# Optimization experiments

Hardware: AMD Instinct MI355X
Metric: run time of the kernel (lower is better)

The kernel has to match this reference:

```python
import jax, jax.numpy as jnp
import numpy as np

N_NODES = 100000
NEG_SLOPE = 0.01  # F.leaky_relu default


def _gin_mean_layer(x, src, dst):
    """DGL GINConv(aggregator='mean', apply_func=None, eps=0, activation=leaky_relu).
    out = leaky_relu((1+eps)*x + mean_{in-neighbors} x_src), nodes with no in-edges get mean=0.
    """
    msg_sum = jax.ops.segment_sum(x[src], dst, num_segments=N_NODES)  # [N, D]
    deg = jax.ops.segment_sum(jnp.ones(src.shape, dtype=x.dtype), dst, num_segments=N_NODES)  # [N]
    mean = msg_sum / jnp.maximum(deg, 1.0)[:, None]
    return jax.nn.leaky_relu(x + mean, negative_slope=NEG_SLOPE)


def setup_inputs() -> dict:
    key = jax.random.key(0)
    k0, k1, k2, k3, k4 = jax.random.split(key, 5)
    n_edges = 640000
    d = 128
    return {
        "node_features": jax.random.normal(k0, (N_NODES, d), dtype=jnp.float32),
        "edges1_src": jax.random.randint(k1, (n_edges,), 0, N_NODES, dtype=jnp.int64),
        "edges1_dst": jax.random.randint(k2, (n_edges,), 0, N_NODES, dtype=jnp.int64),
        "edges2_src": jax.random.randint(k3, (n_edges,), 0, N_NODES, dtype=jnp.int64),
        "edges2_dst": jax.random.randint(k4, (n_edges,), 0, N_NODES, dtype=jnp.int64),
    }


def reference(node_features, edges1_src, edges1_dst, edges2_src, edges2_dst):
    h_AC1 = _gin_mean_layer(node_features, edges1_src, edges1_dst)
    h_CA1 = _gin_mean_layer(node_features, edges2_src, edges2_dst)
    h = jnp.concatenate((h_AC1, h_CA1), axis=1)  # [N, 2D]
    h_AC2 = _gin_mean_layer(h, edges1_src, edges1_dst)
    h_CA2 = _gin_mean_layer(h, edges2_src, edges2_dst)
    return jnp.concatenate((h_AC2, h_CA2), axis=1)  # [N, 4D]
```

## Files before the change

kernel.cpp:

```cpp
#include <hip/hip_runtime.h>

#define N_NODES 100000
#define NEG 0.01f
#define CAP 32
#define EDGE_ILP 8

typedef float f4v __attribute__((ext_vector_type(4)));

__device__ __forceinline__ float lrelu(float v) { return v > 0.f ? v : NEG * v; }

__device__ __forceinline__ unsigned int f2bf(float f) {
    unsigned int x = __float_as_uint(f);
    return (x + 0x7fffu + ((x >> 16) & 1u)) >> 16;
}
__device__ __forceinline__ unsigned int pack2bf(float lo, float hi) {
    return f2bf(lo) | (f2bf(hi) << 16);
}
__device__ __forceinline__ float bf_lo(unsigned int u) { return __uint_as_float(u << 16); }
__device__ __forceinline__ float bf_hi(unsigned int u) { return __uint_as_float(u & 0xffff0000u); }

__device__ __forceinline__ void unpack8(uint4 u, float* f) {
    f[0] = bf_lo(u.x); f[1] = bf_hi(u.x);
    f[2] = bf_lo(u.y); f[3] = bf_hi(u.y);
    f[4] = bf_lo(u.z); f[5] = bf_hi(u.z);
    f[6] = bf_lo(u.w); f[7] = bf_hi(u.w);
}

__device__ __forceinline__ unsigned int packq(float v, int sh) {
    float c = fminf(fmaxf(v * 16.f, -127.f), 127.f);
    int q = __float2int_rn(c);
    return ((unsigned int)(q & 255)) << sh;
}
__device__ __forceinline__ uint2 pack8i8(const float* f) {
    uint2 r;
    r.x = packq(f[0], 0) | packq(f[1], 8) | packq(f[2], 16) | packq(f[3], 24);
    r.y = packq(f[4], 0) | packq(f[5], 8) | packq(f[6], 16) | packq(f[7], 24);
    return r;
}
__device__ __forceinline__ void addsext8(uint2 u, int* acc) {
    acc[0] += ((int)(u.x << 24)) >> 24;
    acc[1] += ((int)(u.x << 16)) >> 24;
    acc[2] += ((int)(u.x <<  8)) >> 24;
    acc[3] += ((int)u.x) >> 24;
    acc[4] += ((int)(u.y << 24)) >> 24;
    acc[5] += ((int)(u.y << 16)) >> 24;
    acc[6] += ((int)(u.y <<  8)) >> 24;
    acc[7] += ((int)u.y) >> 24;
}

__global__ void __launch_bounds__(256) build_and_convert(
        const int* __restrict__ s1, const int* __restrict__ d1a, int E1,
        const int* __restrict__ s2, const int* __restrict__ d2a, int E2,
        int* __restrict__ deg1, int* __restrict__ slots1,
        int* __restrict__ deg2, int* __restrict__ slots2,
        const float4* __restrict__ x, uint4* __restrict__ xb,
        uint2* __restrict__ xi8, int edgeBlocks, int edgeThreads) {
    int b = blockIdx.x;
    if (b < edgeBlocks) {
        int tid = b * 256 + threadIdx.x;
        int E = E1 + E2;
        #pragma unroll
        for (int k = 0; k < EDGE_ILP; ++k) {
            int e = tid + k * edgeThreads;
            if (e < E1) {
                int d = d1a[e];
                int pos = atomicAdd(&deg1[d], 1);
                if (pos < CAP) slots1[d * CAP + pos] = s1[e];
            } else if (e < E) {
                int q = e - E1;
                int d = d2a[q];
                int pos = atomicAdd(&deg2[d], 1);
                if (pos < CAP) slots2[d * CAP + pos] = s2[q];
            }
        }
    } else {
        int i = (b - edgeBlocks) * 256 + threadIdx.x;
        if (i >= N_NODES * 16) return;
        float4 v0 = x[2 * i];
        float4 v1 = x[2 * i + 1];
        uint4 p;
        p.x = pack2bf(v0.x, v0.y);
        p.y = pack2bf(v0.z, v0.w);
        p.z = pack2bf(v1.x, v1.y);
        p.w = pack2bf(v1.z, v1.w);
        xb[i] = p;
        float f[8] = {v0.x, v0.y, v0.z, v0.w, v1.x, v1.y, v1.z, v1.w};
        xi8[i] = pack8i8(f);
    }
}

__global__ void __launch_bounds__(256) layer1(
        const uint4* __restrict__ x4, const uint2* __restrict__ xi8,
        const int* __restrict__ deg1, const int* __restrict__ slots1,
        const int* __restrict__ deg2, const int* __restrict__ slots2,
        uint4* __restrict__ h4, uint2* __restrict__ hi8) {
    int gid = blockIdx.x * blockDim.x + threadIdx.x;
    int n = gid >> 6;
    if (n >= N_NODES) return;
    int lane = gid & 63;
    int t = lane & 15;
    int g = lane >> 4;
    int lane31 = lane & 31;

    int d1 = deg1[n], d2 = deg2[n];
    int v1 = slots1[n * CAP + lane31];
    int v2 = slots2[n * CAP + lane31];
    uint4 xv = x4[(size_t)n * 16 + t];

    int m1 = min(d1, CAP), m2 = min(d2, CAP);

    int sel = (lane < 32) ? v1 : v2;
    int m_own = (g < 2) ? m1 : m2;
    int base = (g < 2) ? 0 : 32;
    int sub = g & 1;
    int L = max((m1 + 1) >> 1, (m2 + 1) >> 1);

    int acc[8] = {0, 0, 0, 0, 0, 0, 0, 0};

    int jj0 = sub, jj1 = sub + 2;
    int s0 = __shfl(sel, base + jj0);
    int s1 = __shfl(sel, base + jj1);
    uint2 u0 = make_uint2(0u, 0u);
    uint2 u1 = make_uint2(0u, 0u);
    if (jj0 < m_own) u0 = xi8[(size_t)s0 * 16 + t];
    if (jj1 < m_own) u1 = xi8[(size_t)s1 * 16 + t];
    for (int i = 0; i < L; ++i) {
        uint2 cur = u0; u0 = u1;
        int jn = 2 * (i + 2) + sub;
        int sn = __shfl(sel, (base + jn) & 63);
        u1 = make_uint2(0u, 0u);
        if (jn < m_own) u1 = xi8[(size_t)sn * 16 + t];
        addsext8(cur, acc);
    }

    #pragma unroll
    for (int i8 = 0; i8 < 8; ++i8) acc[i8] += __shfl_xor(acc[i8], 16);

    float xf[8]; unpack8(xv, xf);
    float r = (g < 2) ? 1.f / (float)max(d1, 1) : 1.f / (float)max(d2, 1);
    float s = r * 0.0625f;

    float o[8];
    #pragma unroll
    for (int i8 = 0; i8 < 8; ++i8) o[i8] = lrelu(xf[i8] + (float)acc[i8] * s);

    if (g == 0) {
        uint4 ob;
        ob.x = pack2bf(o[0], o[1]); ob.y = pack2bf(o[2], o[3]);
        ob.z = pack2bf(o[4], o[5]); ob.w = pack2bf(o[6], o[7]);
        h4[(size_t)n * 32 + t] = ob;
    } else if (g == 2) {
        uint4 ob;
        ob.x = pack2bf(o[0], o[1]); ob.y = pack2bf(o[2], o[3]);
        ob.z = pack2bf(o[4], o[5]); ob.w = pack2bf(o[6], o[7]);
        h4[(size_t)n * 32 + 16 + t] = ob;
    } else if (g == 1) {
        hi8[(size_t)n * 32 + t] = pack8i8(o);
    } else {
        hi8[(size_t)n * 32 + 16 + t] = pack8i8(o);
    }
}

__global__ void __launch_bounds__(256) layer2(
        const uint4* __restrict__ h4, const uint2* __restrict__ hi8,
        const int* __restrict__ deg1, const int* __restrict__ slots1,
        const int* __restrict__ deg2, const int* __restrict__ slots2,
        float4* __restrict__ out4) {
    int gid = blockIdx.x * blockDim.x + threadIdx.x;
    int n = gid >> 6;
    if (n >= N_NODES) return;
    int lane = gid & 63;
    int t = lane & 31;
    int g = lane >> 5;
    int lane31 = lane & 31;

    int d1 = deg1[n], d2 = deg2[n];
    int v1 = slots1[n * CAP + lane31];
    int v2 = slots2[n * CAP + lane31];
    uint4 hv = h4[(size_t)n * 32 + t];

    int m1 = min(d1, CAP), m2 = min(d2, CAP);

    int sel = (lane < 32) ? v1 : v2;
    int m_own = (g == 0) ? m1 : m2;
    int base = g << 5;
    int L = max(m1, m2);

    int acc[8] = {0, 0, 0, 0, 0, 0, 0, 0};

    int s0 = __shfl(sel, base);
    int s1 = __shfl(sel, base + 1);
    uint2 u0 = make_uint2(0u, 0u);
    uint2 u1 = make_uint2(0u, 0u);
    if (0 < m_own) u0 = hi8[(size_t)s0 * 32 + t];
    if (1 < m_own) u1 = hi8[(size_t)s1 * 32 + t];
    for (int i = 0; i < L; ++i) {
        uint2 cur = u0; u0 = u1;
        int jn = i + 2;
        int sn = __shfl(sel, (base + jn) & 63);
        u1 = make_uint2(0u, 0u);
        if (jn < m_own) u1 = hi8[(size_t)sn * 32 + t];
        addsext8(cur, acc);
    }

    float hf[8]; unpack8(hv, hf);
    float r = (g == 0) ? 1.f / (float)max(d1, 1) : 1.f / (float)max(d2, 1);
    float s = r * 0.0625f;

    f4v* ob = (f4v*)out4;
    f4v O0 = {lrelu(hf[0] + (float)acc[0] * s), lrelu(hf[1] + (float)acc[1] * s),
              lrelu(hf[2] + (float)acc[2] * s), lrelu(hf[3] + (float)acc[3] * s)};
    f4v O1 = {lrelu(hf[4] + (float)acc[4] * s), lrelu(hf[5] + (float)acc[5] * s),
              lrelu(hf[6] + (float)acc[6] * s), lrelu(hf[7] + (float)acc[7] * s)};
    size_t off = (size_t)n * 128 + (size_t)g * 64 + 2 * t;
    __builtin_nontemporal_store(O0, &ob[off]);
    __builtin_nontemporal_store(O1, &ob[off + 1]);
}

extern "C" void kernel_launch(void* const* d_in, const int* in_sizes, int n_in,
                              void* d_out, int out_size, void* d_ws, size_t ws_size,
                              hipStream_t stream) {
    const float* x = (const float*)d_in[0];
    const int* e1s = (const int*)d_in[1];
    const int* e1d = (const int*)d_in[2];
    const int* e2s = (const int*)d_in[3];
    const int* e2d = (const int*)d_in[4];
    const int E1 = in_sizes[1];
    const int E2 = in_sizes[3];
    float* out = (float*)d_out;

    int* deg1   = (int*)d_ws;
    int* deg2   = deg1 + N_NODES;
    int* slots1 = deg2 + N_NODES;
    int* slots2 = slots1 + (size_t)N_NODES * CAP;
    unsigned int* xb = (unsigned int*)(slots2 + (size_t)N_NODES * CAP);
    unsigned int* hb = xb + (size_t)N_NODES * 64;
    uint2* hi8 = (uint2*)(hb + (size_t)N_NODES * 128);
    uint2* xi8 = hi8 + (size_t)N_NODES * 32;

    hipMemsetAsync(deg1, 0, 2ull * N_NODES * sizeof(int), stream);

    int convBlocks = (N_NODES * 16 + 255) / 256;
    int edgeThreads = ((E1 + E2 + EDGE_ILP - 1) / EDGE_ILP + 255) / 256 * 256;
    int edgeBlocks = edgeThreads / 256;
    build_and_convert<<<edgeBlocks + convBlocks, 256, 0, stream>>>(
        e1s, e1d, E1, e2s, e2d, E2, deg1, slots1, deg2, slots2,
        (const float4*)x, (uint4*)xb, xi8, edgeBlocks, edgeThreads);

    int blocks = (N_NODES + 3) / 4;
    layer1<<<blocks, 256, 0, stream>>>(
        (const uint4*)xb, xi8, deg1, slots1, deg2, slots2, (uint4*)hb, hi8);
    layer2<<<blocks, 256, 0, stream>>>(
        (const uint4*)hb, hi8, deg1, slots1, deg2, slots2, (float4*)out);
}
```

Measured before the change: 434.1 us.

## Fuse memset, build, and both layers into one cooperative persistent kernel

Replaces the memset plus three kernel launches with a single cooperative kernel of 1024 blocks that uses grid-wide syncs between the phases: zeroing degrees, building the adjacency and converting features, layer 1, and layer 2. Nodes are processed in grid-stride loops, one wave per node. This removes launch overhead and the gaps between kernels. In exchange, occupancy is capped by the fixed grid, each grid.sync has its own cost, and the edge phase depends on edgeBlocks fitting within GRID_BLOCKS (edge ILP 8 over 1.28M edges gives 625 blocks, so the conversion phase gets the remaining 399).

```diff
diff --git a/kernel.cpp b/kernel.cpp
--- a/kernel.cpp
+++ b/kernel.cpp
@@ -1,9 +1,13 @@
 #include <hip/hip_runtime.h>
+#include <hip/hip_cooperative_groups.h>
+
+namespace cg = cooperative_groups;
 
 #define N_NODES 100000
 #define NEG 0.01f
 #define CAP 32
 #define EDGE_ILP 8
+#define GRID_BLOCKS 1024
 
 typedef float f4v __attribute__((ext_vector_type(4)));
 
@@ -48,20 +52,31 @@
     acc[7] += ((int)u.y) >> 24;
 }
 
-__global__ void __launch_bounds__(256) build_and_convert(
+__global__ void __launch_bounds__(256) mega(
         const int* __restrict__ s1, const int* __restrict__ d1a, int E1,
         const int* __restrict__ s2, const int* __restrict__ d2a, int E2,
         int* __restrict__ deg1, int* __restrict__ slots1,
         int* __restrict__ deg2, int* __restrict__ slots2,
         const float4* __restrict__ x, uint4* __restrict__ xb,
-        uint2* __restrict__ xi8, int edgeBlocks, int edgeThreads) {
-    int b = blockIdx.x;
-    if (b < edgeBlocks) {
-        int tid = b * 256 + threadIdx.x;
+        uint2* __restrict__ xi8, uint4* __restrict__ h4,
+        uint2* __restrict__ hi8, float4* __restrict__ out4,
+        int edgeBlocks, int edgeThreads) {
+    cg::grid_group grid = cg::this_grid();
+    const int tid = blockIdx.x * 256 + threadIdx.x;
+    const int nthreads = GRID_BLOCKS * 256;
+    const int lane = tid & 63;
+    const int wid = tid >> 6;
+    const int nwaves = nthreads >> 6;
+
+    for (int i = tid; i < 2 * N_NODES; i += nthreads) deg1[i] = 0;
+    grid.sync();
+
+    if (blockIdx.x < edgeBlocks) {
+        int btid = tid;
         int E = E1 + E2;
         #pragma unroll
         for (int k = 0; k < EDGE_ILP; ++k) {
-            int e = tid + k * edgeThreads;
+            int e = btid + k * edgeThreads;
             if (e < E1) {
                 int d = d1a[e];
                 int pos = atomicAdd(&deg1[d], 1);
@@ -74,160 +89,146 @@
             }
         }
     } else {
-        int i = (b - edgeBlocks) * 256 + threadIdx.x;
-        if (i >= N_NODES * 16) return;
-        float4 v0 = x[2 * i];
-        float4 v1 = x[2 * i + 1];
-        uint4 p;
-        p.x = pack2bf(v0.x, v0.y);
-        p.y = pack2bf(v0.z, v0.w);
-        p.z = pack2bf(v1.x, v1.y);
-        p.w = pack2bf(v1.z, v1.w);
-        xb[i] = p;
-        float f[8] = {v0.x, v0.y, v0.z, v0.w, v1.x, v1.y, v1.z, v1.w};
-        xi8[i] = pack8i8(f);
+        int i0 = (blockIdx.x - edgeBlocks) * 256 + threadIdx.x;
+        int stride = (GRID_BLOCKS - edgeBlocks) * 256;
+        for (int i = i0; i < N_NODES * 16; i += stride) {
+            float4 v0 = x[2 * i];
+            float4 v1 = x[2 * i + 1];
+            uint4 p;
+            p.x = pack2bf(v0.x, v0.y);
+            p.y = pack2bf(v0.z, v0.w);
+            p.z = pack2bf(v1.x, v1.y);
+            p.w = pack2bf(v1.z, v1.w);
+            xb[i] = p;
+            float f[8] = {v0.x, v0.y, v0.z, v0.w, v1.x, v1.y, v1.z, v1.w};
+            xi8[i] = pack8i8(f);
+        }
     }
-}
-
-__global__ void __launch_bounds__(256) layer1(
-        const uint4* __restrict__ x4, const uint2* __restrict__ xi8,
-        const int* __restrict__ deg1, const int* __restrict__ slots1,
-        const int* __restrict__ deg2, const int* __restrict__ slots2,
-        uint4* __restrict__ h4, uint2* __restrict__ hi8) {
-    int gid = blockIdx.x * blockDim.x + threadIdx.x;
-    int n = gid >> 6;
-    if (n >= N_NODES) return;
-    int lane = gid & 63;
-    int t = lane & 15;
-    int g = lane >> 4;
-    int lane31 = lane & 31;
-
-    int d1 = deg1[n], d2 = deg2[n];
-    int v1 = slots1[n * CAP + lane31];
-    int v2 = slots2[n * CAP + lane31];
-    uint4 xv = x4[(size_t)n * 16 + t];
-
-    int m1 = min(d1, CAP), m2 = min(d2, CAP);
-
-    int sel = (lane < 32) ? v1 : v2;
-    int m_own = (g < 2) ? m1 : m2;
-    int base = (g < 2) ? 0 : 32;
-    int sub = g & 1;
-    int L = max((m1 + 1) >> 1, (m2 + 1) >> 1);
-
-    int acc[8] = {0, 0, 0, 0, 0, 0, 0, 0};
-
-    int jj0 = sub, jj1 = sub + 2;
-    int s0 = __shfl(sel, base + jj0);
-    int s1 = __shfl(sel, base + jj1);
-    uint2 u0 = make_uint2(0u, 0u);
-    uint2 u1 = make_uint2(0u, 0u);
-    if (jj0 < m_own) u0 = xi8[(size_t)s0 * 16 + t];
-    if (jj1 < m_own) u1 = xi8[(size_t)s1 * 16 + t];
-    for (int i = 0; i < L; ++i) {
-        uint2 cur = u0; u0 = u1;
-        int jn = 2 * (i + 2) + sub;
-        int sn = __shfl(sel, (base + jn) & 63);
-        u1 = make_uint2(0u, 0u);
-        if (jn < m_own) u1 = xi8[(size_t)sn * 16 + t];
-        addsext8(cur, acc);
+    grid.sync();
+
+    {
+        int t = lane & 15;
+        int g = lane >> 4;
+        int lane31 = lane & 31;
+        for (int n = wid; n < N_NODES; n += nwaves) {
+            int d1 = deg1[n], d2 = deg2[n];
+            int v1 = slots1[n * CAP + lane31];
+            int v2 = slots2[n * CAP + lane31];
+            uint4 xv = xb[(size_t)n * 16 + t];
+
+            int m1 = min(d1, CAP), m2 = min(d2, CAP);
+            int sel = (lane < 32) ? v1 : v2;
+            int m_own = (g < 2) ? m1 : m2;
+            int base = (g < 2) ? 0 : 32;
+            int sub = g & 1;
+            int L = max((m1 + 1) >> 1, (m2 + 1) >> 1);
+
+            int acc[8] = {0, 0, 0, 0, 0, 0, 0, 0};
+
+            int jj0 = sub, jj1 = sub + 2;
+            int s0 = __shfl(sel, base + jj0);
+            int s1v = __shfl(sel, base + jj1);
+            uint2 u0 = make_uint2(0u, 0u);
+            uint2 u1 = make_uint2(0u, 0u);
+            if (jj0 < m_own) u0 = xi8[(size_t)s0 * 16 + t];
+            if (jj1 < m_own) u1 = xi8[(size_t)s1v * 16 + t];
+            for (int i = 0; i < L; ++i) {
+                uint2 cur = u0; u0 = u1;
+                int jn = 2 * (i + 2) + sub;
+                int sn = __shfl(sel, (base + jn) & 63);
+                u1 = make_uint2(0u, 0u);
+                if (jn < m_own) u1 = xi8[(size_t)sn * 16 + t];
+                addsext8(cur, acc);
+            }
+
+            #pragma unroll
+            for (int i8 = 0; i8 < 8; ++i8) acc[i8] += __shfl_xor(acc[i8], 16);
+
+            float xf[8]; unpack8(xv, xf);
+            float r = (g < 2) ? 1.f / (float)max(d1, 1) : 1.f / (float)max(d2, 1);
+            float s = r * 0.0625f;
+
+            float o[8];
+            #pragma unroll
+            for (int i8 = 0; i8 < 8; ++i8) o[i8] = lrelu(xf[i8] + (float)acc[i8] * s);
+
+            if (g == 0) {
+                uint4 ob;
+                ob.x = pack2bf(o[0], o[1]); ob.y = pack2bf(o[2], o[3]);
+                ob.z = pack2bf(o[4], o[5]); ob.w = pack2bf(o[6], o[7]);
+                h4[(size_t)n * 32 + t] = ob;
+            } else if (g == 2) {
+                uint4 ob;
+                ob.x = pack2bf(o[0], o[1]); ob.y = pack2bf(o[2], o[3]);
+                ob.z = pack2bf(o[4], o[5]); ob.w = pack2bf(o[6], o[7]);
+                h4[(size_t)n * 32 + 16 + t] = ob;
+            } else if (g == 1) {
+                hi8[(size_t)n * 32 + t] = pack8i8(o);
+            } else {
+                hi8[(size_t)n * 32 + 16 + t] = pack8i8(o);
+            }
+        }
     }
-
-    #pragma unroll
-    for (int i8 = 0; i8 < 8; ++i8) acc[i8] += __shfl_xor(acc[i8], 16);
-
-    float xf[8]; unpack8(xv, xf);
-    float r = (g < 2) ? 1.f / (float)max(d1, 1) : 1.f / (float)max(d2, 1);
-    float s = r * 0.0625f;
-
-    float o[8];
-    #pragma unroll
-    for (int i8 = 0; i8 < 8; ++i8) o[i8] = lrelu(xf[i8] + (float)acc[i8] * s);
-
-    if (g == 0) {
-        uint4 ob;
-        ob.x = pack2bf(o[0], o[1]); ob.y = pack2bf(o[2], o[3]);
-        ob.z = pack2bf(o[4], o[5]); ob.w = pack2bf(o[6], o[7]);
-        h4[(size_t)n * 32 + t] = ob;
-    } else if (g == 2) {
-        uint4 ob;
-        ob.x = pack2bf(o[0], o[1]); ob.y = pack2bf(o[2], o[3]);
-        ob.z = pack2bf(o[4], o[5]); ob.w = pack2bf(o[6], o[7]);
-        h4[(size_t)n * 32 + 16 + t] = ob;
-    } else if (g == 1) {
-        hi8[(size_t)n * 32 + t] = pack8i8(o);
-    } else {
-        hi8[(size_t)n * 32 + 16 + t] = pack8i8(o);
+    grid.sync();
+
+    {
+        int t = lane & 31;
+        int g = lane >> 5;
+        int lane31 = lane & 31;
+        f4v* ob = (f4v*)out4;
+        for (int n = wid; n < N_NODES; n += nwaves) {
+            int d1 = deg1[n], d2 = deg2[n];
+            int v1 = slots1[n * CAP + lane31];
+            int v2 = slots2[n * CAP + lane31];
+            uint4 hv = h4[(size_t)n * 32 + t];
+
+            int m1 = min(d1, CAP), m2 = min(d2, CAP);
+            int sel = (lane < 32) ? v1 : v2;
+            int m_own = (g == 0) ? m1 : m2;
+            int base = g << 5;
+            int L = max(m1, m2);
+
+            int acc[8] = {0, 0, 0, 0, 0, 0, 0, 0};
+
+            int s0 = __shfl(sel, base);
+            int s1v = __shfl(sel, base + 1);
+            uint2 u0 = make_uint2(0u, 0u);
+            uint2 u1 = make_uint2(0u, 0u);
+            if (0 < m_own) u0 = hi8[(size_t)s0 * 32 + t];
+            if (1 < m_own) u1 = hi8[(size_t)s1v * 32 + t];
+            for (int i = 0; i < L; ++i) {
+                uint2 cur = u0; u0 = u1;
+                int jn = i + 2;
+                int sn = __shfl(sel, (base + jn) & 63);
+                u1 = make_uint2(0u, 0u);
+                if (jn < m_own) u1 = hi8[(size_t)sn * 32 + t];
+                addsext8(cur, acc);
+            }
+
+            float hf[8]; unpack8(hv, hf);
+            float r = (g == 0) ? 1.f / (float)max(d1, 1) : 1.f / (float)max(d2, 1);
+            float s = r * 0.0625f;
+
+            f4v O0 = {lrelu(hf[0] + (float)acc[0] * s), lrelu(hf[1] + (float)acc[1] * s),
+                      lrelu(hf[2] + (float)acc[2] * s), lrelu(hf[3] + (float)acc[3] * s)};
+            f4v O1 = {lrelu(hf[4] + (float)acc[4] * s), lrelu(hf[5] + (float)acc[5] * s),
+                      lrelu(hf[6] + (float)acc[6] * s), lrelu(hf[7] + (float)acc[7] * s)};
+            size_t off = (size_t)n * 128 + (size_t)g * 64 + 2 * t;
+            __builtin_nontemporal_store(O0, &ob[off]);
+            __builtin_nontemporal_store(O1, &ob[off + 1]);
+        }
     }
-}
-
-__global__ void __launch_bounds__(256) layer2(
-        const uint4* __restrict__ h4, const uint2* __restrict__ hi8,
-        const int* __restrict__ deg1, const int* __restrict__ slots1,
-        const int* __restrict__ deg2, const int* __restrict__ slots2,
-        float4* __restrict__ out4) {
-    int gid = blockIdx.x * blockDim.x + threadIdx.x;
-    int n = gid >> 6;
-    if (n >= N_NODES) return;
-    int lane = gid & 63;
-    int t = lane & 31;
-    int g = lane >> 5;
-    int lane31 = lane & 31;
-
-    int d1 = deg1[n], d2 = deg2[n];
-    int v1 = slots1[n * CAP + lane31];
-    int v2 = slots2[n * CAP + lane31];
-    uint4 hv = h4[(size_t)n * 32 + t];
-
-    int m1 = min(d1, CAP), m2 = min(d2, CAP);
-
-    int sel = (lane < 32) ? v1 : v2;
-    int m_own = (g == 0) ? m1 : m2;
-    int base = g << 5;
-    int L = max(m1, m2);
-
-    int acc[8] = {0, 0, 0, 0, 0, 0, 0, 0};
-
-    int s0 = __shfl(sel, base);
-    int s1 = __shfl(sel, base + 1);
-    uint2 u0 = make_uint2(0u, 0u);
-    uint2 u1 = make_uint2(0u, 0u);
-    if (0 < m_own) u0 = hi8[(size_t)s0 * 32 + t];
-    if (1 < m_own) u1 = hi8[(size_t)s1 * 32 + t];
-    for (int i = 0; i < L; ++i) {
-        uint2 cur = u0; u0 = u1;
-        int jn = i + 2;
-        int sn = __shfl(sel, (base + jn) & 63);
-        u1 = make_uint2(0u, 0u);
-        if (jn < m_own) u1 = hi8[(size_t)sn * 32 + t];
-        addsext8(cur, acc);
-    }
-
-    float hf[8]; unpack8(hv, hf);
-    float r = (g == 0) ? 1.f / (float)max(d1, 1) : 1.f / (float)max(d2, 1);
-    float s = r * 0.0625f;
-
-    f4v* ob = (f4v*)out4;
-    f4v O0 = {lrelu(hf[0] + (float)acc[0] * s), lrelu(hf[1] + (float)acc[1] * s),
-              lrelu(hf[2] + (float)acc[2] * s), lrelu(hf[3] + (float)acc[3] * s)};
-    f4v O1 = {lrelu(hf[4] + (float)acc[4] * s), lrelu(hf[5] + (float)acc[5] * s),
-              lrelu(hf[6] + (float)acc[6] * s), lrelu(hf[7] + (float)acc[7] * s)};
-    size_t off = (size_t)n * 128 + (size_t)g * 64 + 2 * t;
-    __builtin_nontemporal_store(O0, &ob[off]);
-    __builtin_nontemporal_store(O1, &ob[off + 1]);
 }
 
 extern "C" void kernel_launch(void* const* d_in, const int* in_sizes, int n_in,
                               void* d_out, int out_size, void* d_ws, size_t ws_size,
                               hipStream_t stream) {
-    const float* x = (const float*)d_in[0];
     const int* e1s = (const int*)d_in[1];
     const int* e1d = (const int*)d_in[2];
     const int* e2s = (const int*)d_in[3];
     const int* e2d = (const int*)d_in[4];
-    const int E1 = in_sizes[1];
-    const int E2 = in_sizes[3];
-    float* out = (float*)d_out;
+    int E1 = in_sizes[1];
+    int E2 = in_sizes[3];
 
     int* deg1   = (int*)d_ws;
     int* deg2   = deg1 + N_NODES;
@@ -238,18 +239,22 @@
     uint2* hi8 = (uint2*)(hb + (size_t)N_NODES * 128);
     uint2* xi8 = hi8 + (size_t)N_NODES * 32;
 
-    hipMemsetAsync(deg1, 0, 2ull * N_NODES * sizeof(int), stream);
-
-    int convBlocks = (N_NODES * 16 + 255) / 256;
-    int edgeThreads = ((E1 + E2 + EDGE_ILP - 1) / EDGE_ILP + 255) / 256 * 256;
+    const float4* xp = (const float4*)d_in[0];
+    uint4* xbp = (uint4*)xb;
+    uint4* h4p = (uint4*)hb;
+    float4* outp = (float4*)d_out;
+
+    int E = E1 + E2;
+    int edgeThreads = ((E + EDGE_ILP - 1) / EDGE_ILP + 255) / 256 * 256;
     int edgeBlocks = edgeThreads / 256;
-    build_and_convert<<<edgeBlocks + convBlocks, 256, 0, stream>>>(
-        e1s, e1d, E1, e2s, e2d, E2, deg1, slots1, deg2, slots2,
-        (const float4*)x, (uint4*)xb, xi8, edgeBlocks, edgeThreads);
-
-    int blocks = (N_NODES + 3) / 4;
-    layer1<<<blocks, 256, 0, stream>>>(
-        (const uint4*)xb, xi8, deg1, slots1, deg2, slots2, (uint4*)hb, hi8);
-    layer2<<<blocks, 256, 0, stream>>>(
-        (const uint4*)hb, hi8, deg1, slots1, deg2, slots2, (float4*)out);
-}
+
+    void* args[] = {
+        (void*)&e1s, (void*)&e1d, (void*)&E1,
+        (void*)&e2s, (void*)&e2d, (void*)&E2,
+        (void*)&deg1, (void*)&slots1, (void*)&deg2, (void*)&slots2,
+        (void*)&xp, (void*)&xbp, (void*)&xi8, (void*)&h4p, (void*)&hi8,
+        (void*)&outp, (void*)&edgeBlocks, (void*)&edgeThreads,
+    };
+    hipLaunchCooperativeKernel((const void*)mega, dim3(GRID_BLOCKS), dim3(256),
+                               args, 0, stream);
+}
```

Result: slower. 764.6 us (+76.1%).
